# Performance work log

Measured on AMD Instinct MI355X. Metric: run time of the kernel, lower is better.

Reference implementation:

```python
import jax, jax.numpy as jnp
import numpy as np

N_ADAPTERS = 16
RANK = 16
ALPHA = 16.0
SCALING = ALPHA / RANK
B, S, IN, OUT = 32, 512, 1024, 4096


def setup_inputs() -> dict:
    key = jax.random.key(0)
    k1, k2, k3, k4, k5, k6 = jax.random.split(key, 6)
    hidden_states = jax.random.normal(k1, (B, S, IN), dtype=jnp.float32)
    adapter_ids = jax.random.randint(k2, (B,), 0, N_ADAPTERS, dtype=jnp.int64)
    W = jax.random.normal(k3, (IN, OUT), dtype=jnp.float32) * 0.02
    b = jax.random.normal(k4, (OUT,), dtype=jnp.float32) * 0.02
    lora_a = jax.random.normal(k5, (N_ADAPTERS, IN, RANK), dtype=jnp.float32) * (1.0 / np.sqrt(IN))
    lora_b = jax.random.normal(k6, (N_ADAPTERS, RANK, OUT), dtype=jnp.float32) * 0.02
    return {"hidden_states": hidden_states, "adapter_ids": adapter_ids,
            "W": W, "b": b, "lora_a": lora_a, "lora_b": lora_b}


def reference(hidden_states, adapter_ids, W, b, lora_a, lora_b):
    # Base Conv1D (GPT-2 style): x @ W + b  -> [B, S, OUT]
    base_output = jnp.einsum('bsi,io->bso', hidden_states, W) + b
    # Per-sample adapter gather (replaces the unique-id loop + boolean masks):
    a_sel = lora_a[adapter_ids]          # [B, IN, R]
    b_sel = lora_b[adapter_ids]          # [B, R, OUT]
    low_rank = jnp.einsum('bsi,bir->bsr', hidden_states, a_sel)   # [B, S, R]
    delta = jnp.einsum('bsr,bro->bso', low_rank, b_sel) * SCALING # [B, S, OUT]
    return base_output + delta
```

## Files before the change

kernel.cpp:

```cpp
#include <hip/hip_runtime.h>

#define M_TOT 16384
#define N_TOT 4096
#define K_TOT 1024
#define R_LORA 16

#define BM 256
#define BN 256
#define BK 64
#define NT (K_TOT / BK)

typedef __attribute__((ext_vector_type(8))) short bf16x8_t;
typedef __attribute__((ext_vector_type(4))) float f32x4_t;

__device__ __forceinline__ unsigned short f2bf(float f) {
  unsigned u = __builtin_bit_cast(unsigned, f);
  u += 0x7FFFu + ((u >> 16) & 1u);
  return (unsigned short)(u >> 16);
}

__device__ __forceinline__ void gload_lds16(const void* g, void* l) {
  __builtin_amdgcn_global_load_lds(
      (const __attribute__((address_space(1))) unsigned int*)g,
      (__attribute__((address_space(3))) unsigned int*)l, 16, 0, 0);
}

__global__ __launch_bounds__(256) void prep_kernel(const float* __restrict__ x,
                                                   const float* __restrict__ W,
                                                   const float* __restrict__ lora_a,
                                                   const float* __restrict__ lora_b,
                                                   unsigned short* __restrict__ xB,
                                                   unsigned short* __restrict__ WtB,
                                                   unsigned short* __restrict__ AtB,
                                                   unsigned short* __restrict__ lbT) {
  __shared__ float lds[64][65];
  const int bid = blockIdx.x;
  const int t = threadIdx.x;
  if (bid < 1024) {
    size_t i = (size_t)bid * 256 + t;
    const size_t stride = (size_t)1024 * 256;
    const size_t n4 = (size_t)M_TOT * K_TOT / 4;
    for (; i < n4; i += stride) {
      float4 v = ((const float4*)x)[i];
      ushort4 h;
      h.x = f2bf(v.x); h.y = f2bf(v.y); h.z = f2bf(v.z); h.w = f2bf(v.w);
      ((ushort4*)xB)[i] = h;
    }
  } else if (bid < 2048) {
    const int v = bid - 1024;
    const int k0 = (v & 15) * 64;
    const int n0 = (v >> 4) * 64;
    const int rr = t >> 4;
    const int cc = (t & 15) * 4;
#pragma unroll
    for (int i = 0; i < 4; ++i) {
      int row = i * 16 + rr;
      float4 w4 = *(const float4*)(W + (size_t)(k0 + row) * N_TOT + n0 + cc);
      lds[row][cc + 0] = w4.x; lds[row][cc + 1] = w4.y;
      lds[row][cc + 2] = w4.z; lds[row][cc + 3] = w4.w;
    }
    __syncthreads();
#pragma unroll
    for (int i = 0; i < 4; ++i) {
      int nrow = i * 16 + rr;
      ushort4 h;
      h.x = f2bf(lds[cc + 0][nrow]); h.y = f2bf(lds[cc + 1][nrow]);
      h.z = f2bf(lds[cc + 2][nrow]); h.w = f2bf(lds[cc + 3][nrow]);
      *(ushort4*)(WtB + (size_t)(n0 + nrow) * K_TOT + k0 + cc) = h;
    }
  } else {
    const int b2 = bid - 2048;
    if (b2 < 64) {
      int idx = b2 * 256 + t;
      int aid = idx >> 10;
      int k = idx & 1023;
      const float* src = lora_a + (size_t)idx * 16;
#pragma unroll
      for (int q = 0; q < 4; ++q) {
        float4 v4 = ((const float4*)src)[q];
#pragma unroll
        for (int j = 0; j < 4; ++j) {
          int r = q * 4 + j;
          float val = (j == 0) ? v4.x : (j == 1) ? v4.y : (j == 2) ? v4.z : v4.w;
          AtB[(((size_t)aid * 16 + r) << 10) + k] = f2bf(val);
        }
      }
    } else {
      int idx = (b2 - 64) * 256 + t;
      int aid = idx >> 12;
      int n = idx & 4095;
      unsigned short o[16];
#pragma unroll
      for (int r = 0; r < 16; ++r)
        o[r] = f2bf(lora_b[((size_t)aid * 16 + r) * N_TOT + n]);
      ushort4* dst = (ushort4*)(lbT + ((size_t)aid * N_TOT + n) * 16);
#pragma unroll
      for (int q = 0; q < 4; ++q) {
        ushort4 h; h.x = o[q*4+0]; h.y = o[q*4+1]; h.z = o[q*4+2]; h.w = o[q*4+3];
        dst[q] = h;
      }
    }
  }
}

__global__ __launch_bounds__(256) void lowrank_kernel(const unsigned short* __restrict__ xB,
                                                      const unsigned short* __restrict__ AtB,
                                                      const int* __restrict__ aids,
                                                      unsigned short* __restrict__ lrB) {
  __shared__ char As[128 * 128];
  const int blk = blockIdx.x;
  const int t = threadIdx.x;
  const int lane = t & 63;
  const int w = t >> 6;
  const int fr = lane & 15, fq = lane >> 4;
  const int aid = aids[blk >> 2];

  const unsigned short* aSrc[4];
  char* aDst[4];
#pragma unroll
  for (int r = 0; r < 4; ++r) {
    int off = (r * 256 + t) * 16;
    int row = off >> 7, cb = off & 127;
    int sb = cb ^ ((row & 7) << 4);
    aSrc[r] = xB + (size_t)(blk * 128 + row) * K_TOT + (sb >> 1);
    aDst[r] = As + off;
  }
  const unsigned short* bBase = AtB + ((size_t)aid * 16 + fr) * K_TOT + fq * 8;

  f32x4_t acc[2];
  acc[0] = (f32x4_t){0.f, 0.f, 0.f, 0.f};
  acc[1] = (f32x4_t){0.f, 0.f, 0.f, 0.f};

  for (int kt = 0; kt < K_TOT / 64; ++kt) {
#pragma unroll
    for (int r = 0; r < 4; ++r) gload_lds16(aSrc[r] + kt * 64, aDst[r]);
    __syncthreads();
#pragma unroll
    for (int ks = 0; ks < 2; ++ks) {
      bf16x8_t bfr = *(const bf16x8_t*)(bBase + kt * 64 + ks * 32);
#pragma unroll
      for (int m = 0; m < 2; ++m) {
        int row = w * 32 + m * 16 + fr;
        int cb = ks * 64 + fq * 16;
        bf16x8_t af = *(const bf16x8_t*)(As + row * 128 + (cb ^ ((row & 7) << 4)));
        acc[m] = __builtin_amdgcn_mfma_f32_16x16x32_bf16(af, bfr, acc[m], 0, 0, 0);
      }
    }
    __syncthreads();
  }
#pragma unroll
  for (int m = 0; m < 2; ++m) {
    int gm0 = blk * 128 + w * 32 + m * 16 + fq * 4;
#pragma unroll
    for (int q = 0; q < 4; ++q)
      lrB[(size_t)(gm0 + q) * R_LORA + fr] = f2bf(acc[m][q]);
  }
}

#define BAR() __builtin_amdgcn_s_barrier()
#define WAIT_LGKM0() asm volatile("s_waitcnt lgkmcnt(0)" ::: "memory")

#define STAGE_HALF(gbase, koff, ldsbase)                                   \
  do {                                                                     \
    gload_lds16((const char*)(gbase) + (koff), (ldsbase) + t * 16);        \
    gload_lds16((const char*)(gbase) + 64 * 2048 + (koff),                 \
                (ldsbase) + 8192 + t * 16);                                \
  } while (0)

#define LDA(MH)                                                            \
  do {                                                                     \
    _Pragma("unroll") for (int m = 0; m < 4; ++m)                          \
      _Pragma("unroll") for (int ks = 0; ks < 2; ++ks)                     \
        aF[m][ks] = *(const bf16x8_t*)(bufA + (MH) * 8192 + m * 2048 +     \
                                       (laneA ^ (ks << 6)));               \
  } while (0)

#define LDB(NH)                                                            \
  do {                                                                     \
    _Pragma("unroll") for (int n = 0; n < 2; ++n)                          \
      _Pragma("unroll") for (int ks = 0; ks < 2; ++ks)                     \
        bF[NH][n][ks] = *(const bf16x8_t*)(bufB + (NH) * 4096 + n * 2048 + \
                                           (laneA ^ (ks << 6)));           \
  } while (0)

#define MM(MH, NH)                                                         \
  do {                                                                     \
    __builtin_amdgcn_s_setprio(1);                                         \
    _Pragma("unroll") for (int ks = 0; ks < 2; ++ks)                       \
      _Pragma("unroll") for (int m = 0; m < 4; ++m)                        \
        _Pragma("unroll") for (int n = 0; n < 2; ++n)                      \
          acc[(MH) * 4 + m][(NH) * 2 + n] =                                \
              __builtin_amdgcn_mfma_f32_16x16x32_bf16(                     \
                  aF[m][ks], bF[NH][n][ks],                                \
                  acc[(MH) * 4 + m][(NH) * 2 + n], 0, 0, 0);               \
    __builtin_amdgcn_s_setprio(0);                                         \
  } while (0)

__global__ __launch_bounds__(512, 1) void gemm_kernel(
    const unsigned short* __restrict__ xB, const unsigned short* __restrict__ WtB,
    const unsigned short* __restrict__ lrB, const unsigned short* __restrict__ lbT,
    const float* __restrict__ bias, const int* __restrict__ aids,
    float* __restrict__ out) {
  __shared__ char smem[131072];

  const int orig = blockIdx.x;
  const int wg = (orig & 7) * 128 + (orig >> 3);
  const int tn = wg & 15;
  const int tm = wg >> 4;

  const int t = threadIdx.x;
  const int lane = t & 63;
  const int wid = t >> 6;
  const int wr = wid >> 2;
  const int wc = wid & 3;
  const int fr = lane & 15, fq = lane >> 4;

  const int laneA = fr * 128 + (((fq << 4) ^ ((fr & 7) << 4)));
  const int waveAoff = wr * 16384;
  const int waveBoff = 32768 + (wc >> 1) * 16384 + (wc & 1) * 8192;

  const int srow = t >> 3;
  const int sb = (((t & 7) ^ (srow & 7)) << 4);
  const char* pAsrc0 = (const char*)xB + (size_t)(tm * 256 + srow) * 2048 + sb;
  const char* pAsrc1 = pAsrc0 + (size_t)128 * 2048;
  const char* pBsrc0 = (const char*)WtB + (size_t)(tn * 256 + srow) * 2048 + sb;
  const char* pBsrc1 = pBsrc0 + (size_t)128 * 2048;

  f32x4_t acc[8][4];
#pragma unroll
  for (int m = 0; m < 8; ++m)
#pragma unroll
    for (int n = 0; n < 4; ++n) acc[m][n] = (f32x4_t){0.f, 0.f, 0.f, 0.f};

  bf16x8_t aF[4][2];
  bf16x8_t bF[2][2][2];

  STAGE_HALF(pAsrc0, 0, smem + 0);
  STAGE_HALF(pAsrc1, 0, smem + 16384);
  STAGE_HALF(pBsrc0, 0, smem + 32768);
  STAGE_HALF(pBsrc1, 0, smem + 49152);
  STAGE_HALF(pBsrc0, 128, smem + 65536 + 32768);
  STAGE_HALF(pBsrc1, 128, smem + 65536 + 49152);
  asm volatile("s_waitcnt vmcnt(4)" ::: "memory");
  BAR();

#pragma unroll 1
  for (int kt = 0; kt < NT; ++kt) {
    char* base = smem + ((kt & 1) << 16);
    char* nbase = smem + (((kt + 1) & 1) << 16);
    char* bufA = base + waveAoff;
    char* bufB = base + waveBoff;
    const int kb1 = (kt + 1) * 128;
    const int kb2 = (kt + 2) * 128;

    LDA(0);
    LDB(0);
    if (kt + 1 < NT) STAGE_HALF(pAsrc0, kb1, nbase + 0);
    asm volatile("s_waitcnt lgkmcnt(8)" ::: "memory");
    BAR(); WAIT_LGKM0();
    MM(0, 0);
    BAR();

    LDB(1);
    if (kt + 1 < NT) STAGE_HALF(pAsrc1, kb1, nbase + 16384);
    BAR(); WAIT_LGKM0();
    MM(0, 1);
    BAR();

    LDA(1);
    if (kt + 2 < NT) STAGE_HALF(pBsrc0, kb2, base + 32768);
    BAR(); WAIT_LGKM0();
    MM(1, 1);
    BAR();

    if (kt + 2 < NT) STAGE_HALF(pBsrc1, kb2, base + 49152);
    BAR(); WAIT_LGKM0();
    MM(1, 0);
    if (kt < NT - 2) asm volatile("s_waitcnt vmcnt(4)" ::: "memory");
    else             asm volatile("s_waitcnt vmcnt(0)" ::: "memory");
    BAR();
  }

  const int aid = aids[tm >> 1];
  bf16x8_t z8 = (bf16x8_t){0, 0, 0, 0, 0, 0, 0, 0};
  bf16x8_t lrf[8], lbf[4];
#pragma unroll
  for (int m = 0; m < 8; ++m) lrf[m] = z8;
#pragma unroll
  for (int n = 0; n < 4; ++n) lbf[n] = z8;
  if (fq < 2) {
#pragma unroll
    for (int m = 0; m < 8; ++m)
      lrf[m] = *(const bf16x8_t*)(lrB + (size_t)(tm * 256 + wr * 128 + m * 16 + fr) * R_LORA + fq * 8);
#pragma unroll
    for (int n = 0; n < 4; ++n)
      lbf[n] = *(const bf16x8_t*)(lbT + ((size_t)aid * N_TOT + tn * 256 + wc * 64 + n * 16 + fr) * R_LORA + fq * 8);
  }
#pragma unroll
  for (int m = 0; m < 8; ++m)
#pragma unroll
    for (int n = 0; n < 4; ++n)
      acc[m][n] = __builtin_amdgcn_mfma_f32_16x16x32_bf16(lrf[m], lbf[n], acc[m][n], 0, 0, 0);

#pragma unroll
  for (int n = 0; n < 4; ++n) {
    int gn = tn * 256 + wc * 64 + n * 16 + fr;
    float bv = bias[gn];
#pragma unroll
    for (int m = 0; m < 8; ++m) {
      int gm0 = tm * 256 + wr * 128 + m * 16 + fq * 4;
      float* op = out + (size_t)gm0 * N_TOT + gn;
#pragma unroll
      for (int q = 0; q < 4; ++q) op[(size_t)q * N_TOT] = acc[m][n][q] + bv;
    }
  }
}

extern "C" void kernel_launch(void* const* d_in, const int* in_sizes, int n_in,
                              void* d_out, int out_size, void* d_ws, size_t ws_size,
                              hipStream_t stream) {
  const float* x      = (const float*)d_in[0];
  const int*   aids   = (const int*)d_in[1];
  const float* W      = (const float*)d_in[2];
  const float* bias   = (const float*)d_in[3];
  const float* lora_a = (const float*)d_in[4];
  const float* lora_b = (const float*)d_in[5];
  float* out = (float*)d_out;

  char* ws = (char*)d_ws;
  unsigned short* xB  = (unsigned short*)(ws);
  unsigned short* WtB = (unsigned short*)(ws + (size_t)32 * 1024 * 1024);
  unsigned short* lrB = (unsigned short*)(ws + (size_t)40 * 1024 * 1024);
  unsigned short* AtB = (unsigned short*)(ws + (size_t)40 * 1024 * 1024 + 512 * 1024);
  unsigned short* lbT = (unsigned short*)(ws + (size_t)41 * 1024 * 1024);

  prep_kernel<<<2368, 256, 0, stream>>>(x, W, lora_a, lora_b, xB, WtB, AtB, lbT);
  lowrank_kernel<<<128, 256, 0, stream>>>(xB, AtB, aids, lrB);
  gemm_kernel<<<1024, 512, 0, stream>>>(xB, WtB, lrB, lbT, bias, aids, out);
}
```

Measured before the change: 213.3 us.

## Make GEMM persistent over four N tiles per block with continuous pipeline

Each workgroup now handles four consecutive 256-wide N tiles for one M tile, for 256 blocks instead of 1024. The K loop runs continuously across tiles, so the double-buffered prefetch of the next tile's B overlaps the epilogue of the current tile. This removes the pipeline ramp-up and drain between tiles. Launch bounds were also changed to request two blocks per CU, but 128KB of LDS per block likely still allows only one, and with 256 blocks some CUs may sit idle or the load may balance poorly.

```diff
diff --git a/kernel.cpp b/kernel.cpp
--- a/kernel.cpp
+++ b/kernel.cpp
@@ -8,7 +8,7 @@
 #define BM 256
 #define BN 256
 #define BK 64
-#define NT (K_TOT / BK)
+#define NSTEP 64
 
 typedef __attribute__((ext_vector_type(8))) short bf16x8_t;
 typedef __attribute__((ext_vector_type(4))) float f32x4_t;
@@ -196,7 +196,7 @@
     __builtin_amdgcn_s_setprio(0);                                         \
   } while (0)
 
-__global__ __launch_bounds__(512, 1) void gemm_kernel(
+__global__ __launch_bounds__(512, 2) void gemm_kernel(
     const unsigned short* __restrict__ xB, const unsigned short* __restrict__ WtB,
     const unsigned short* __restrict__ lrB, const unsigned short* __restrict__ lbT,
     const float* __restrict__ bias, const int* __restrict__ aids,
@@ -204,9 +204,9 @@
   __shared__ char smem[131072];
 
   const int orig = blockIdx.x;
-  const int wg = (orig & 7) * 128 + (orig >> 3);
-  const int tn = wg & 15;
-  const int tm = wg >> 4;
+  const int wg = (orig & 7) * 32 + (orig >> 3);
+  const int tm = wg & 63;
+  const int tn0 = (wg >> 6) * 4;
 
   const int t = threadIdx.x;
   const int lane = t & 63;
@@ -223,8 +223,7 @@
   const int sb = (((t & 7) ^ (srow & 7)) << 4);
   const char* pAsrc0 = (const char*)xB + (size_t)(tm * 256 + srow) * 2048 + sb;
   const char* pAsrc1 = pAsrc0 + (size_t)128 * 2048;
-  const char* pBsrc0 = (const char*)WtB + (size_t)(tn * 256 + srow) * 2048 + sb;
-  const char* pBsrc1 = pBsrc0 + (size_t)128 * 2048;
+  const char* pBbase = (const char*)WtB + (size_t)srow * 2048 + sb;
 
   f32x4_t acc[8][4];
 #pragma unroll
@@ -235,83 +234,102 @@
   bf16x8_t aF[4][2];
   bf16x8_t bF[2][2][2];
 
-  STAGE_HALF(pAsrc0, 0, smem + 0);
-  STAGE_HALF(pAsrc1, 0, smem + 16384);
-  STAGE_HALF(pBsrc0, 0, smem + 32768);
-  STAGE_HALF(pBsrc1, 0, smem + 49152);
-  STAGE_HALF(pBsrc0, 128, smem + 65536 + 32768);
-  STAGE_HALF(pBsrc1, 128, smem + 65536 + 49152);
+  {
+    const char* pB0 = pBbase + (size_t)tn0 * 256 * 2048;
+    STAGE_HALF(pAsrc0, 0, smem + 0);
+    STAGE_HALF(pAsrc1, 0, smem + 16384);
+    STAGE_HALF(pB0, 0, smem + 32768);
+    STAGE_HALF(pB0 + (size_t)128 * 2048, 0, smem + 49152);
+    STAGE_HALF(pB0, 128, smem + 65536 + 32768);
+    STAGE_HALF(pB0 + (size_t)128 * 2048, 128, smem + 65536 + 49152);
+  }
   asm volatile("s_waitcnt vmcnt(4)" ::: "memory");
   BAR();
 
 #pragma unroll 1
-  for (int kt = 0; kt < NT; ++kt) {
-    char* base = smem + ((kt & 1) << 16);
-    char* nbase = smem + (((kt + 1) & 1) << 16);
+  for (int s = 0; s < NSTEP; ++s) {
+    char* base = smem + ((s & 1) << 16);
+    char* nbase = smem + (((s + 1) & 1) << 16);
     char* bufA = base + waveAoff;
     char* bufB = base + waveBoff;
-    const int kb1 = (kt + 1) * 128;
-    const int kb2 = (kt + 2) * 128;
+    const int ka1 = ((s + 1) & 15) * 128;
+    const bool stA = (s + 1 < NSTEP);
+    const bool stB = (s + 2 < NSTEP);
+    const char* pBs = pBbase;
+    int kb2 = 0;
+    if (stB) {
+      int s2 = s + 2;
+      pBs = pBbase + (size_t)(tn0 + (s2 >> 4)) * 256 * 2048;
+      kb2 = (s2 & 15) * 128;
+    }
 
     LDA(0);
     LDB(0);
-    if (kt + 1 < NT) STAGE_HALF(pAsrc0, kb1, nbase + 0);
+    if (stA) STAGE_HALF(pAsrc0, ka1, nbase + 0);
     asm volatile("s_waitcnt lgkmcnt(8)" ::: "memory");
     BAR(); WAIT_LGKM0();
     MM(0, 0);
     BAR();
 
     LDB(1);
-    if (kt + 1 < NT) STAGE_HALF(pAsrc1, kb1, nbase + 16384);
+    if (stA) STAGE_HALF(pAsrc1, ka1, nbase + 16384);
     BAR(); WAIT_LGKM0();
     MM(0, 1);
     BAR();
 
     LDA(1);
-    if (kt + 2 < NT) STAGE_HALF(pBsrc0, kb2, base + 32768);
+    if (stB) STAGE_HALF(pBs, kb2, base + 32768);
     BAR(); WAIT_LGKM0();
     MM(1, 1);
     BAR();
 
-    if (kt + 2 < NT) STAGE_HALF(pBsrc1, kb2, base + 49152);
+    if (stB) STAGE_HALF(pBs + (size_t)128 * 2048, kb2, base + 49152);
     BAR(); WAIT_LGKM0();
     MM(1, 0);
-    if (kt < NT - 2) asm volatile("s_waitcnt vmcnt(4)" ::: "memory");
-    else             asm volatile("s_waitcnt vmcnt(0)" ::: "memory");
+    if (s < NSTEP - 2) asm volatile("s_waitcnt vmcnt(4)" ::: "memory");
+    else               asm volatile("s_waitcnt vmcnt(0)" ::: "memory");
     BAR();
-  }
-
-  const int aid = aids[tm >> 1];
-  bf16x8_t z8 = (bf16x8_t){0, 0, 0, 0, 0, 0, 0, 0};
-  bf16x8_t lrf[8], lbf[4];
-#pragma unroll
-  for (int m = 0; m < 8; ++m) lrf[m] = z8;
-#pragma unroll
-  for (int n = 0; n < 4; ++n) lbf[n] = z8;
-  if (fq < 2) {
-#pragma unroll
-    for (int m = 0; m < 8; ++m)
-      lrf[m] = *(const bf16x8_t*)(lrB + (size_t)(tm * 256 + wr * 128 + m * 16 + fr) * R_LORA + fq * 8);
-#pragma unroll
-    for (int n = 0; n < 4; ++n)
-      lbf[n] = *(const bf16x8_t*)(lbT + ((size_t)aid * N_TOT + tn * 256 + wc * 64 + n * 16 + fr) * R_LORA + fq * 8);
-  }
-#pragma unroll
-  for (int m = 0; m < 8; ++m)
-#pragma unroll
-    for (int n = 0; n < 4; ++n)
-      acc[m][n] = __builtin_amdgcn_mfma_f32_16x16x32_bf16(lrf[m], lbf[n], acc[m][n], 0, 0, 0);
-
-#pragma unroll
-  for (int n = 0; n < 4; ++n) {
-    int gn = tn * 256 + wc * 64 + n * 16 + fr;
-    float bv = bias[gn];
-#pragma unroll
-    for (int m = 0; m < 8; ++m) {
-      int gm0 = tm * 256 + wr * 128 + m * 16 + fq * 4;
-      float* op = out + (size_t)gm0 * N_TOT + gn;
-#pragma unroll
-      for (int q = 0; q < 4; ++q) op[(size_t)q * N_TOT] = acc[m][n][q] + bv;
+
+    if ((s & 15) == 15) {
+      const int j = s >> 4;
+      const int tn = tn0 + j;
+      const int aid = aids[tm >> 1];
+      bf16x8_t z8 = (bf16x8_t){0, 0, 0, 0, 0, 0, 0, 0};
+      bf16x8_t lrf[8], lbf[4];
+#pragma unroll
+      for (int m = 0; m < 8; ++m) lrf[m] = z8;
+#pragma unroll
+      for (int n = 0; n < 4; ++n) lbf[n] = z8;
+      if (fq < 2) {
+#pragma unroll
+        for (int m = 0; m < 8; ++m)
+          lrf[m] = *(const bf16x8_t*)(lrB + (size_t)(tm * 256 + wr * 128 + m * 16 + fr) * R_LORA + fq * 8);
+#pragma unroll
+        for (int n = 0; n < 4; ++n)
+          lbf[n] = *(const bf16x8_t*)(lbT + ((size_t)aid * N_TOT + tn * 256 + wc * 64 + n * 16 + fr) * R_LORA + fq * 8);
+      }
+#pragma unroll
+      for (int m = 0; m < 8; ++m)
+#pragma unroll
+        for (int n = 0; n < 4; ++n)
+          acc[m][n] = __builtin_amdgcn_mfma_f32_16x16x32_bf16(lrf[m], lbf[n], acc[m][n], 0, 0, 0);
+
+#pragma unroll
+      for (int n = 0; n < 4; ++n) {
+        int gn = tn * 256 + wc * 64 + n * 16 + fr;
+        float bv = bias[gn];
+#pragma unroll
+        for (int m = 0; m < 8; ++m) {
+          int gm0 = tm * 256 + wr * 128 + m * 16 + fq * 4;
+          float* op = out + (size_t)gm0 * N_TOT + gn;
+#pragma unroll
+          for (int q = 0; q < 4; ++q) op[(size_t)q * N_TOT] = acc[m][n][q] + bv;
+        }
+      }
+#pragma unroll
+      for (int m = 0; m < 8; ++m)
+#pragma unroll
+        for (int n = 0; n < 4; ++n) acc[m][n] = (f32x4_t){0.f, 0.f, 0.f, 0.f};
     }
   }
 }
@@ -336,5 +354,5 @@
 
   prep_kernel<<<2368, 256, 0, stream>>>(x, W, lora_a, lora_b, xB, WtB, AtB, lbT);
   lowrank_kernel<<<128, 256, 0, stream>>>(xB, AtB, aids, lrB);
-  gemm_kernel<<<1024, 512, 0, stream>>>(xB, WtB, lrB, lbT, bias, aids, out);
-}
+  gemm_kernel<<<256, 512, 0, stream>>>(xB, WtB, lrB, lbT, bias, aids, out);
+}
```

After: 240.1 us. 1.13x slower.

## Load B operand directly from global into registers and halve LDS for two blocks per CU

Applied to the files above, without the earlier changes.

The B (weight) operand is no longer staged through LDS; each wave loads its B fragments straight from global memory into registers, with one half prefetched a step ahead in ping-pong register sets. LDS shrinks to 64KB holding only double-buffered A tiles, and launch bounds allow two workgroups per CU to improve latency hiding. The trade-off is uncoalesced, redundant global reads of W across waves, higher register pressure that could spill with 2 blocks/CU, and a full vmcnt(0) wait every step that may expose global latency.

```diff
diff --git a/kernel.cpp b/kernel.cpp
--- a/kernel.cpp
+++ b/kernel.cpp
@@ -175,15 +175,15 @@
                                        (laneA ^ (ks << 6)));               \
   } while (0)
 
-#define LDB(NH)                                                            \
+#define LOADB(dst, H, kbyte)                                               \
   do {                                                                     \
     _Pragma("unroll") for (int n = 0; n < 2; ++n)                          \
       _Pragma("unroll") for (int ks = 0; ks < 2; ++ks)                     \
-        bF[NH][n][ks] = *(const bf16x8_t*)(bufB + (NH) * 4096 + n * 2048 + \
-                                           (laneA ^ (ks << 6)));           \
-  } while (0)
-
-#define MM(MH, NH)                                                         \
+        dst[n][ks] = *(const bf16x8_t*)(pB + bOff[(H) * 2 + n] + (kbyte) + \
+                                        ks * 64);                          \
+  } while (0)
+
+#define MM(MH, BSET, NH)                                                   \
   do {                                                                     \
     __builtin_amdgcn_s_setprio(1);                                         \
     _Pragma("unroll") for (int ks = 0; ks < 2; ++ks)                       \
@@ -191,17 +191,49 @@
         _Pragma("unroll") for (int n = 0; n < 2; ++n)                      \
           acc[(MH) * 4 + m][(NH) * 2 + n] =                                \
               __builtin_amdgcn_mfma_f32_16x16x32_bf16(                     \
-                  aF[m][ks], bF[NH][n][ks],                                \
+                  aF[m][ks], BSET[n][ks],                                  \
                   acc[(MH) * 4 + m][(NH) * 2 + n], 0, 0, 0);               \
     __builtin_amdgcn_s_setprio(0);                                         \
   } while (0)
 
-__global__ __launch_bounds__(512, 1) void gemm_kernel(
+#define GSTEP(S, B0CUR, B0NXT)                                             \
+  do {                                                                     \
+    char* base = smem + (((S) & 1) << 15);                                 \
+    char* nbase = smem + ((((S) + 1) & 1) << 15);                          \
+    char* bufA = base + waveAoff;                                          \
+    const bool st = ((S) + 1 < NT);                                        \
+    const int ka1 = ((S) + 1) * 128;                                       \
+                            \
+    LDA(0);                                                                \
+    LOADB(b1, 1, (S) * 128);                                               \
+    BAR(); WAIT_LGKM0();                                                   \
+    MM(0, B0CUR, 0);                                                       \
+    BAR();                                                                 \
+                              \
+    if (st) STAGE_HALF(pAsrc0, ka1, nbase + 0);                            \
+    BAR();                                                                 \
+    MM(0, b1, 1);                                                          \
+    BAR();                                                                 \
+                              \
+    LDA(1);                                                                \
+    if (st) STAGE_HALF(pAsrc1, ka1, nbase + 16384);                        \
+    BAR(); WAIT_LGKM0();                                                   \
+    MM(1, b1, 1);                                                          \
+    BAR();                                                                 \
+            \
+    if (st) LOADB(B0NXT, 0, ka1);                                          \
+    BAR();                                                                 \
+    MM(1, B0CUR, 0);                                                       \
+    asm volatile("s_waitcnt vmcnt(0)" ::: "memory");                       \
+    BAR();                                                                 \
+  } while (0)
+
+__global__ __launch_bounds__(512, 2) void gemm_kernel(
     const unsigned short* __restrict__ xB, const unsigned short* __restrict__ WtB,
     const unsigned short* __restrict__ lrB, const unsigned short* __restrict__ lbT,
     const float* __restrict__ bias, const int* __restrict__ aids,
     float* __restrict__ out) {
-  __shared__ char smem[131072];
+  __shared__ char smem[65536];
 
   const int orig = blockIdx.x;
   const int wg = (orig & 7) * 128 + (orig >> 3);
@@ -217,14 +249,20 @@
 
   const int laneA = fr * 128 + (((fq << 4) ^ ((fr & 7) << 4)));
   const int waveAoff = wr * 16384;
-  const int waveBoff = 32768 + (wc >> 1) * 16384 + (wc & 1) * 8192;
 
   const int srow = t >> 3;
   const int sb = (((t & 7) ^ (srow & 7)) << 4);
   const char* pAsrc0 = (const char*)xB + (size_t)(tm * 256 + srow) * 2048 + sb;
   const char* pAsrc1 = pAsrc0 + (size_t)128 * 2048;
-  const char* pBsrc0 = (const char*)WtB + (size_t)(tn * 256 + srow) * 2048 + sb;
-  const char* pBsrc1 = pBsrc0 + (size_t)128 * 2048;
+
+  const char* pB = (const char*)WtB;
+  unsigned bOff[4];
+#pragma unroll
+  for (int h = 0; h < 2; ++h)
+#pragma unroll
+    for (int n = 0; n < 2; ++n)
+      bOff[h * 2 + n] =
+          (unsigned)((tn * 256 + wc * 64 + h * 32 + n * 16 + fr) * 2048 + fq * 16);
 
   f32x4_t acc[8][4];
 #pragma unroll
@@ -233,52 +271,18 @@
     for (int n = 0; n < 4; ++n) acc[m][n] = (f32x4_t){0.f, 0.f, 0.f, 0.f};
 
   bf16x8_t aF[4][2];
-  bf16x8_t bF[2][2][2];
+  bf16x8_t b0a[2][2], b0b[2][2], b1[2][2];
 
   STAGE_HALF(pAsrc0, 0, smem + 0);
   STAGE_HALF(pAsrc1, 0, smem + 16384);
-  STAGE_HALF(pBsrc0, 0, smem + 32768);
-  STAGE_HALF(pBsrc1, 0, smem + 49152);
-  STAGE_HALF(pBsrc0, 128, smem + 65536 + 32768);
-  STAGE_HALF(pBsrc1, 128, smem + 65536 + 49152);
-  asm volatile("s_waitcnt vmcnt(4)" ::: "memory");
+  LOADB(b0a, 0, 0);
+  asm volatile("s_waitcnt vmcnt(0)" ::: "memory");
   BAR();
 
 #pragma unroll 1
-  for (int kt = 0; kt < NT; ++kt) {
-    char* base = smem + ((kt & 1) << 16);
-    char* nbase = smem + (((kt + 1) & 1) << 16);
-    char* bufA = base + waveAoff;
-    char* bufB = base + waveBoff;
-    const int kb1 = (kt + 1) * 128;
-    const int kb2 = (kt + 2) * 128;
-
-    LDA(0);
-    LDB(0);
-    if (kt + 1 < NT) STAGE_HALF(pAsrc0, kb1, nbase + 0);
-    asm volatile("s_waitcnt lgkmcnt(8)" ::: "memory");
-    BAR(); WAIT_LGKM0();
-    MM(0, 0);
-    BAR();
-
-    LDB(1);
-    if (kt + 1 < NT) STAGE_HALF(pAsrc1, kb1, nbase + 16384);
-    BAR(); WAIT_LGKM0();
-    MM(0, 1);
-    BAR();
-
-    LDA(1);
-    if (kt + 2 < NT) STAGE_HALF(pBsrc0, kb2, base + 32768);
-    BAR(); WAIT_LGKM0();
-    MM(1, 1);
-    BAR();
-
-    if (kt + 2 < NT) STAGE_HALF(pBsrc1, kb2, base + 49152);
-    BAR(); WAIT_LGKM0();
-    MM(1, 0);
-    if (kt < NT - 2) asm volatile("s_waitcnt vmcnt(4)" ::: "memory");
-    else             asm volatile("s_waitcnt vmcnt(0)" ::: "memory");
-    BAR();
+  for (int s2 = 0; s2 < NT; s2 += 2) {
+    GSTEP(s2, b0a, b0b);
+    GSTEP(s2 + 1, b0b, b0a);
   }
 
   const int aid = aids[tm >> 1];
```

Measured after the change: 302.3 us. 1.42x slower.
